# Kernel tuning notes

Measured on AMD Instinct MI355X. Metric: run time of the kernel, lower is better.

## Reference

```python
import jax, jax.numpy as jnp
import numpy as np

SIG = [1, 1, 1, 1, -1]  # Cl(4,1)
NVEC = 5
GA = 1 << NVEC  # 32


def _build_gp_table():
    # Cayley table for the geometric product on blades indexed by bitmask.
    G = np.zeros((GA, GA, GA), np.float32)
    for a in range(GA):
        for b in range(GA):
            s = 0
            t = a >> 1
            while t:
                s += bin(t & b).count('1')
                t >>= 1
            sign = -1.0 if (s & 1) else 1.0
            common = a & b
            for i in range(NVEC):
                if (common >> i) & 1:
                    sign *= SIG[i]
            G[a, b, a ^ b] = sign
    return G

GP_TABLE = jnp.asarray(_build_gp_table())


def geometric_product(x, y):
    return jnp.einsum('...i,...j,ijk->...k', x, y, GP_TABLE)


def manifold_norm(x):
    # normalize each multivector onto the unit sphere in R^32
    return x / (jnp.linalg.norm(x, axis=-1, keepdims=True) + 1e-6)


def versor_linear(x, W, b):
    # channel mixing shared across multivector components: x [..., in, ga]
    return jnp.einsum('...ig,oi->...og', x, W) + b


def layer_norm2d(x, w, b):
    # LayerNorm over last two dims [D, ga] jointly
    mu = jnp.mean(x, axis=(-2, -1), keepdims=True)
    var = jnp.var(x, axis=(-2, -1), keepdims=True)
    return (x - mu) / jnp.sqrt(var + 1e-5) * w + b


def attention(x, Wq, bq, Wk, bk, Wv, bv, Wo, bo, n_heads):
    B, S, D, G = x.shape
    dh = D // n_heads
    q = versor_linear(x, Wq, bq).reshape(B, S, n_heads, dh, G)
    k = versor_linear(x, Wk, bk).reshape(B, S, n_heads, dh, G)
    v = versor_linear(x, Wv, bv).reshape(B, S, n_heads, dh, G)
    scale = 1.0 / np.sqrt(dh * G).astype(np.float32)
    scores = jnp.einsum('bshdg,bthdg->bhst', q, k) * scale
    probs = jax.nn.softmax(scores, axis=-1)
    o = jnp.einsum('bhst,bthdg->bshdg', probs, v).reshape(B, S, D, G)
    return versor_linear(o, Wo, bo)


N_HEADS = 8


def forward(x, Wq, bq, Wk, bk, Wv, bv, Wo, bo, ln1_w, ln1_b, ln2_w, ln2_b,
            gamma1, gamma2, W1, b1, W2, b2, Wr, br, Wc, bc):
    L = Wq.shape[0]
    for l in range(L):
        h = attention(layer_norm2d(x, ln1_w[l], ln1_b[l]),
                      Wq[l], bq[l], Wk[l], bk[l], Wv[l], bv[l], Wo[l], bo[l], N_HEADS)
        x = manifold_norm(x + gamma1[l] * h)
        m = versor_linear(layer_norm2d(x, ln2_w[l], ln2_b[l]), W1[l], b1[l])
        m = versor_linear(jnp.tanh(m), W2[l], b2[l])
        x = manifold_norm(x + gamma2[l] * m)
    # RecursiveRotorAccumulator: log(S)-step inclusive scan of rotors
    delta = versor_linear(x, Wr, br)
    rot = 0.5 * delta
    rot = rot.at[..., 0].add(1.0)
    rot = manifold_norm(rot)
    S = x.shape[1]
    step = 1
    while step < S:
        left = rot[:, :-step]
        right = rot[:, step:]
        comb = manifold_norm(geometric_product(right, left))
        rot = jnp.concatenate([rot[:, :step], comb], axis=1)
        step *= 2
    pooled = rot[:, -1]  # [B, D, ga]
    logits = pooled.reshape(pooled.shape[0], -1) @ Wc.T + bc
    return logits


def setup_inputs() -> dict:
    key = jax.random.key(0)
    B, S, D, G, L, NC = 8, 256, 64, GA, 4, 1000
    E = 4 * D  # expansion hidden
    ks = jax.random.split(key, 16)
    sd = 0.02
    inp = {
        'x': jax.random.normal(ks[0], (B, S, D, G), jnp.float32),
        'Wq': jax.random.normal(ks[1], (L, D, D), jnp.float32) * sd,
        'bq': jnp.zeros((L, D, G), jnp.float32),
        'Wk': jax.random.normal(ks[2], (L, D, D), jnp.float32) * sd,
        'bk': jnp.zeros((L, D, G), jnp.float32),
        'Wv': jax.random.normal(ks[3], (L, D, D), jnp.float32) * sd,
        'bv': jnp.zeros((L, D, G), jnp.float32),
        'Wo': jax.random.normal(ks[4], (L, D, D), jnp.float32) * sd,
        'bo': jnp.zeros((L, D, G), jnp.float32),
        'ln1_w': jnp.ones((L, D, G), jnp.float32),
        'ln1_b': jnp.zeros((L, D, G), jnp.float32),
        'ln2_w': jnp.ones((L, D, G), jnp.float32),
        'ln2_b': jnp.zeros((L, D, G), jnp.float32),
        'gamma1': 1e-5 * jnp.ones((L, D, G), jnp.float32),
        'gamma2': 1e-5 * jnp.ones((L, D, G), jnp.float32),
        'W1': jax.random.normal(ks[5], (L, E, D), jnp.float32) * sd,
        'b1': jnp.zeros((L, E, G), jnp.float32),
        'W2': jax.random.normal(ks[6], (L, D, E), jnp.float32) * sd,
        'b2': jnp.zeros((L, D, G), jnp.float32),
        'Wr': jax.random.normal(ks[7], (D, D), jnp.float32) * sd,
        'br': jnp.zeros((D, G), jnp.float32),
        'Wc': jax.random.normal(ks[8], (NC, D * G), jnp.float32) * sd,
        'bc': jnp.zeros((NC,), jnp.float32),
    }
    return inp


def reference(x, Wq, bq, Wk, bk, Wv, bv, Wo, bo, ln1_w, ln1_b, ln2_w, ln2_b,
              gamma1, gamma2, W1, b1, W2, b2, Wr, br, Wc, bc):
    return forward(x, Wq, bq, Wk, bk, Wv, bv, Wo, bo, ln1_w, ln1_b, ln2_w, ln2_b,
                   gamma1, gamma2, W1, b1, W2, b2, Wr, br, Wc, bc)
```

## Files before the change

### kernel.cpp

```cpp
#include <hip/hip_runtime.h>
#include <hip/hip_bf16.h>

constexpr int kB  = 8;
constexpr int kS  = 256;
constexpr int kD  = 64;
constexpr int kG  = 32;
constexpr int kE  = 256;
constexpr int kNH = 8;
constexpr int kHD = 256;
constexpr int kDG = kD * kG;
constexpr int kT  = kB * kS;
constexpr int kNC = 1000;

using bf16x8 = __attribute__((ext_vector_type(8))) short;
using f32x4  = __attribute__((ext_vector_type(4))) float;

__device__ __forceinline__ short f2bf(float f) {
    unsigned u = __float_as_uint(f);
    unsigned r = (u + 0x7FFFu + ((u >> 16) & 1u)) >> 16;
    return (short)r;
}

__device__ __forceinline__ float tanh_fast(float x) {
    float a = fabsf(x);
// ... 60 lines not shown
#pragma unroll
    for (int j = 0; j < 8; j++) {
        float x = xp[tid + j * 256];
        v[j] = x; s += x; ss += x * x;
        int jj = tid + j * 256;
        xf[(jj & 31) * 68 + (jj >> 5)] = x;
    }
    r1[tid] = s; r2[tid] = ss; __syncthreads();
    for (int o = 128; o > 0; o >>= 1) {
        if (tid < o) { r1[tid] += r1[tid + o]; r2[tid] += r2[tid + o]; }
        __syncthreads();
    }
    float mean = r1[0] * (1.f / kDG);
    float var  = r2[0] * (1.f / kDG) - mean * mean;
    float rstd = rsqrtf(var + 1e-5f);
#pragma unroll
    for (int j = 0; j < 8; j++) {
        int jj = tid + j * 256;
        float val = (v[j] - mean) * rstd * w[jj] + b[jj];
        st[(jj & 31) * 72 + (jj >> 5)] = f2bf(val);
    }
    __syncthreads();
    bf16x8 ov = *(const bf16x8*)&st[(tid >> 3) * 72 + (tid & 7) * 8];
    *(bf16x8*)&A[(size_t)t * kDG + tid * 8] = ov;
    const int row = tid >> 3, col = (tid & 7) * 8;
    float* xo = XT + (size_t)t * kDG + tid * 8;
    *(float4*)(xo + 0) = *(const float4*)&xf[row * 68 + col + 0];
    *(float4*)(xo + 4) = *(const float4*)&xf[row * 68 + col + 4];
}

__global__ __launch_bounds__(256) void vlinT_kernel(const float* __restrict__ XT,
                                                    const float* __restrict__ W,
                                                    const float* __restrict__ bias,
                                                    float* __restrict__ OutT) {
    __shared__ float sx[32 * 65];
    __shared__ float sw[kD * kD];
    int t = blockIdx.x, tid = threadIdx.x;
    const float* xp = XT + (size_t)t * kDG;
    for (int j = tid; j < kDG; j += 256) sx[(j >> 6) * 65 + (j & 63)] = xp[j];
    for (int j = tid; j < kD * kD; j += 256) sw[j] = W[j];
    __syncthreads();
    int g = tid & 31, ob = tid >> 5;
    int b = t >> 8, s = t & 255;
    float* op = OutT + ((size_t)b * kD * kS + s) * kG;
    for (int o = ob; o < kD; o += 8) {
        float acc = bias[o * kG + g];
        const float* wr = sw + o * kD;
#pragma unroll
        for (int i = 0; i < kD; i++) acc += wr[i] * sx[g * 65 + i];
        op[(size_t)o * kS * kG + g] = acc;
    }
}

template<bool LAST>
__global__ __launch_bounds__(128, 3) void mega_kernel(
    const unsigned short* __restrict__ O,
    const unsigned short* __restrict__ Woh, const float* __restrict__ boT,
    const float* __restrict__ gm1T,
    const float* __restrict__ ln2wT, const float* __restrict__ ln2bT,
    const unsigned short* __restrict__ W1h, const float* __restrict__ b1T,
    const unsigned short* __restrict__ W2h, const float* __restrict__ b2T,
    const float* __restrict__ gm2T,
    const float* __restrict__ ln1wT, const float* __restrict__ ln1bT,
    float* __restrict__ XT,
    const unsigned short* __restrict__ Wqh, const unsigned short* __restrict__ Wkh,
    const unsigned short* __restrict__ Wvh,
    const float* __restrict__ bqT, const float* __restrict__ bkT,
    const float* __restrict__ bvT,
    unsigned short* __restrict__ Q, unsigned short* __restrict__ K,
    unsigned short* __restrict__ V) {
    constexpr int AS = 72;
    constexpr int MS = 264;
    __shared__ short sA[32 * AS];
    __shared__ short sM[32 * MS];
    __shared__ float sred[4];

    const int tid = threadIdx.x;
    const int w = tid >> 6, lane = tid & 63;
    const int l16 = lane & 15, quad = lane >> 4;
    const int tok = blockIdx.x;
    const size_t tb = (size_t)tok * kDG;

    float xv[2][2][4];
    bf16x8 w1f[8];
    {
        const unsigned short* xp = O + tb;
        bf16x8 bfr[2][2];
#pragma unroll
        for (int c = 0; c < 2; ++c)
#pragma unroll
            for (int nt = 0; nt < 2; ++nt)
                bfr[c][nt] = *(const bf16x8*)&xp[(nt * 16 + l16) * kD + c * 32 + quad * 8];

        f32x4 accW[2][2];
#pragma unroll
        for (int mt = 0; mt < 2; ++mt)
#pragma unroll
            for (int nt = 0; nt < 2; ++nt) accW[mt][nt] = (f32x4){0.f, 0.f, 0.f, 0.f};
#pragma unroll
        for (int mt = 0; mt < 2; ++mt)
#pragma unroll
            for (int c = 0; c < 2; ++c) {
                bf16x8 afr = *(const bf16x8*)&Woh[(w * 32 + mt * 16 + l16) * kD + c * 32 + quad * 8];
#pragma unroll
                for (int nt = 0; nt < 2; ++nt)
                    accW[mt][nt] = __builtin_amdgcn_mfma_f32_16x16x32_bf16(afr, bfr[c][nt], accW[mt][nt], 0, 0, 0);
            }

#pragma unroll
        for (int mt = 0; mt < 4; ++mt)
#pragma unroll
            for (int c = 0; c < 2; ++c)
                w1f[mt * 2 + c] = *(const bf16x8*)&W1h[((w * 8 + mt) * 16 + l16) * kD + c * 32 + quad * 8];

        float s = 0.f, ss = 0.f;
#pragma unroll
        for (int mt = 0; mt < 2; ++mt) {
            int o0 = w * 32 + mt * 16 + quad * 4;
            float vv[2][4];
#pragma unroll
            for (int nt = 0; nt < 2; ++nt) {
                int g = nt * 16 + l16;
                const float4 b4 = *(const float4*)&boT[g * kD + o0];
                const float4 g4 = *(const float4*)&gm1T[g * kD + o0];
                const float4 xi = *(const float4*)&XT[tb + g * kD + o0];
#pragma unroll
                for (int r = 0; r < 4; ++r)
                    vv[nt][r] = (&xi.x)[r] + (&g4.x)[r] * (accW[mt][nt][r] + (&b4.x)[r]);
            }
#pragma unroll
            for (int r = 0; r < 4; ++r) {
                float sq = vv[0][r] * vv[0][r] + vv[1][r] * vv[1][r];
#pragma unroll
                for (int off = 1; off < 16; off <<= 1) sq += __shfl_xor(sq, off, 64);
                float rn = 1.f / (sqrtf(sq) + 1e-6f);
#pragma unroll
                for (int nt = 0; nt < 2; ++nt) {
                    float x = vv[nt][r] * rn;
                    xv[mt][nt][r] = x;
                    s += x; ss = fmaf(x, x, ss);
                }
            }
        }
#pragma unroll
        for (int off = 1; off < 64; off <<= 1) {
            s += __shfl_xor(s, off, 64); ss += __shfl_xor(ss, off, 64);
        }
        if (lane == 0) { sred[w] = s; sred[2 + w] = ss; }
        __syncthreads();
        float st = sred[0] + sred[1], sst = sred[2] + sred[3];
        float mean = st * (1.f / kDG);
        float var  = sst * (1.f / kDG) - mean * mean;
        float rstd = rsqrtf(var + 1e-5f);
#pragma unroll
        for (int mt = 0; mt < 2; ++mt)
#pragma unroll
            for (int nt = 0; nt < 2; ++nt) {
                int g = nt * 16 + l16;
                int o0 = w * 32 + mt * 16 + quad * 4;
                const float4 w4 = *(const float4*)&ln2wT[g * kD + o0];
                const float4 b4 = *(const float4*)&ln2bT[g * kD + o0];
                short4 s4;
#pragma unroll
                for (int r = 0; r < 4; ++r)
                    (&s4.x)[r] = f2bf((xv[mt][nt][r] - mean) * rstd * (&w4.x)[r] + (&b4.x)[r]);
                *(short4*)&sA[g * AS + o0] = s4;
            }
    }
    __syncthreads();

    bf16x8 w2f[16];
    {
        bf16x8 afrA[2][2];
#pragma unroll
        for (int c = 0; c < 2; ++c)
#pragma unroll
            for (int nt = 0; nt < 2; ++nt)
                afrA[c][nt] = *(const bf16x8*)&sA[(nt * 16 + l16) * AS + c * 32 + quad * 8];

        f32x4 acc1[4][2];
#pragma unroll
        for (int mt = 0; mt < 4; ++mt)
#pragma unroll
            for (int nt = 0; nt < 2; ++nt) acc1[mt][nt] = (f32x4){0.f, 0.f, 0.f, 0.f};
#pragma unroll
        for (int mt = 0; mt < 4; ++mt)
#pragma unroll
            for (int c = 0; c < 2; ++c)
#pragma unroll
                for (int nt = 0; nt < 2; ++nt)
                    acc1[mt][nt] = __builtin_amdgcn_mfma_f32_16x16x32_bf16(w1f[mt * 2 + c], afrA[c][nt], acc1[mt][nt], 0, 0, 0);

        bf16x8 w1g[8];
#pragma unroll
        for (int mt = 0; mt < 4; ++mt)
#pragma unroll
            for (int c = 0; c < 2; ++c)
                w1g[mt * 2 + c] = *(const bf16x8*)&W1h[((w * 8 + 4 + mt) * 16 + l16) * kD + c * 32 + quad * 8];

#pragma unroll
        for (int mt = 0; mt < 4; ++mt)
#pragma unroll
            for (int nt = 0; nt < 2; ++nt) {
                int g = nt * 16 + l16;
                int e0 = (w * 8 + mt) * 16 + quad * 4;
                const float4 b4 = *(const float4*)&b1T[g * kE + e0];
                short4 s4;
#pragma unroll
                for (int r = 0; r < 4; ++r)
                    (&s4.x)[r] = f2bf(tanh_fast(acc1[mt][nt][r] + (&b4.x)[r]));
                *(short4*)&sM[g * MS + e0] = s4;
            }

        f32x4 acc1b[4][2];
#pragma unroll
        for (int mt = 0; mt < 4; ++mt)
#pragma unroll
            for (int nt = 0; nt < 2; ++nt) acc1b[mt][nt] = (f32x4){0.f, 0.f, 0.f, 0.f};
#pragma unroll
        for (int mt = 0; mt < 4; ++mt)
#pragma unroll
            for (int c = 0; c < 2; ++c)
#pragma unroll
                for (int nt = 0; nt < 2; ++nt)
                    acc1b[mt][nt] = __builtin_amdgcn_mfma_f32_16x16x32_bf16(w1g[mt * 2 + c], afrA[c][nt], acc1b[mt][nt], 0, 0, 0);

#pragma unroll
        for (int mt = 0; mt < 2; ++mt)
#pragma unroll
            for (int c = 0; c < 8; ++c)
                w2f[mt * 8 + c] = *(const bf16x8*)&W2h[(w * 32 + mt * 16 + l16) * kE + c * 32 + quad * 8];

#pragma unroll
        for (int mt = 0; mt < 4; ++mt)
#pragma unroll
            for (int nt = 0; nt < 2; ++nt) {
                int g = nt * 16 + l16;
                int e0 = (w * 8 + 4 + mt) * 16 + quad * 4;
                const float4 b4 = *(const float4*)&b1T[g * kE + e0];
                short4 s4;
#pragma unroll
                for (int r = 0; r < 4; ++r)
                    (&s4.x)[r] = f2bf(tanh_fast(acc1b[mt][nt][r] + (&b4.x)[r]));
                *(short4*)&sM[g * MS + e0] = s4;
            }
    }
    __syncthreads();

    f32x4 acc2[2][2];
#pragma unroll
    for (int mt = 0; mt < 2; ++mt)
#pragma unroll
        for (int nt = 0; nt < 2; ++nt) acc2[mt][nt] = (f32x4){0.f, 0.f, 0.f, 0.f};
#pragma unroll
    for (int c = 0; c < 8; ++c) {
        bf16x8 bq[2];
#pragma unroll
        for (int nt = 0; nt < 2; ++nt)
            bq[nt] = *(const bf16x8*)&sM[(nt * 16 + l16) * MS + c * 32 + quad * 8];
#pragma unroll
        for (int mt = 0; mt < 2; ++mt)
#pragma unroll
            for (int nt = 0; nt < 2; ++nt)
                acc2[mt][nt] = __builtin_amdgcn_mfma_f32_16x16x32_bf16(w2f[mt * 8 + c], bq[nt], acc2[mt][nt], 0, 0, 0);
    }

    bf16x8 wqf[12];
    if constexpr (!LAST) {
        const unsigned short* Wp[3] = {Wqh, Wkh, Wvh};
#pragma unroll
        for (int m = 0; m < 3; ++m)
#pragma unroll
            for (int mt = 0; mt < 2; ++mt)
#pragma unroll
                for (int c = 0; c < 2; ++c)
                    wqf[m * 4 + mt * 2 + c] = *(const bf16x8*)&Wp[m][(w * 32 + mt * 16 + l16) * kD + c * 32 + quad * 8];
    }

    float yv[2][2][4];
    float s2 = 0.f, ss2 = 0.f;
#pragma unroll
    for (int mt = 0; mt < 2; ++mt) {
        int o0 = w * 32 + mt * 16 + quad * 4;
        float vv[2][4];
#pragma unroll
        for (int nt = 0; nt < 2; ++nt) {
            int g = nt * 16 + l16;
            const float4 b4 = *(const float4*)&b2T[g * kD + o0];
            const float4 g4 = *(const float4*)&gm2T[g * kD + o0];
#pragma unroll
            for (int r = 0; r < 4; ++r)
                vv[nt][r] = xv[mt][nt][r] + (&g4.x)[r] * (acc2[mt][nt][r] + (&b4.x)[r]);
        }
#pragma unroll
        for (int r = 0; r < 4; ++r) {
            float sq = vv[0][r] * vv[0][r] + vv[1][r] * vv[1][r];
#pragma unroll
            for (int off = 1; off < 16; off <<= 1) sq += __shfl_xor(sq, off, 64);
            float rn = 1.f / (sqrtf(sq) + 1e-6f);
#pragma unroll
            for (int nt = 0; nt < 2; ++nt) {
                float x = vv[nt][r] * rn;
                yv[mt][nt][r] = x;
                s2 += x; ss2 = fmaf(x, x, ss2);
            }
        }
#pragma unroll
        for (int nt = 0; nt < 2; ++nt) {
            int g = nt * 16 + l16;
            float4 xo;
#pragma unroll
            for (int r = 0; r < 4; ++r) (&xo.x)[r] = yv[mt][nt][r];
            *(float4*)&XT[tb + g * kD + o0] = xo;
        }
    }
    if constexpr (LAST) return;

#pragma unroll
    for (int off = 1; off < 64; off <<= 1) {
        s2 += __shfl_xor(s2, off, 64); ss2 += __shfl_xor(ss2, off, 64);
    }
    if (lane == 0) { sred[w] = s2; sred[2 + w] = ss2; }
    __syncthreads();
    {
        float st = sred[0] + sred[1], sst = sred[2] + sred[3];
        float mean = st * (1.f / kDG);
        float var  = sst * (1.f / kDG) - mean * mean;
        float rstd = rsqrtf(var + 1e-5f);
#pragma unroll
        for (int mt = 0; mt < 2; ++mt)
#pragma unroll
            for (int nt = 0; nt < 2; ++nt) {
                int g = nt * 16 + l16;
                int o0 = w * 32 + mt * 16 + quad * 4;
                const float4 w4 = *(const float4*)&ln1wT[g * kD + o0];
                const float4 b4 = *(const float4*)&ln1bT[g * kD + o0];
                short4 s4;
#pragma unroll
                for (int r = 0; r < 4; ++r)
                    (&s4.x)[r] = f2bf((yv[mt][nt][r] - mean) * rstd * (&w4.x)[r] + (&b4.x)[r]);
                *(short4*)&sA[g * AS + o0] = s4;
            }
    }
    __syncthreads();

    {
        bf16x8 afrA[2][2];
#pragma unroll
        for (int c = 0; c < 2; ++c)
#pragma unroll
            for (int nt = 0; nt < 2; ++nt)
                afrA[c][nt] = *(const bf16x8*)&sA[(nt * 16 + l16) * AS + c * 32 + quad * 8];

        const float* Bp[3] = {bqT, bkT, bvT};
        unsigned short* Op[3] = {Q, K, V};
#pragma unroll
        for (int m = 0; m < 3; ++m) {
            f32x4 acc3[2][2];
#pragma unroll
            for (int mt = 0; mt < 2; ++mt)
#pragma unroll
                for (int nt = 0; nt < 2; ++nt) acc3[mt][nt] = (f32x4){0.f, 0.f, 0.f, 0.f};
#pragma unroll
            for (int mt = 0; mt < 2; ++mt)
#pragma unroll
                for (int c = 0; c < 2; ++c)
#pragma unroll
                    for (int nt = 0; nt < 2; ++nt)
                        acc3[mt][nt] = __builtin_amdgcn_mfma_f32_16x16x32_bf16(wqf[m * 4 + mt * 2 + c], afrA[c][nt], acc3[mt][nt], 0, 0, 0);
            unsigned short* op = Op[m] + tb;
#pragma unroll
            for (int mt = 0; mt < 2; ++mt)
#pragma unroll
                for (int nt = 0; nt < 2; ++nt) {
                    int g = nt * 16 + l16;
                    int o0 = w * 32 + mt * 16 + quad * 4;
                    const float4 b4 = *(const float4*)&Bp[m][g * kD + o0];
#pragma unroll
                    for (int r = 0; r < 4; ++r)
                        op[(o0 + r) * kG + g] = (unsigned short)f2bf(acc3[mt][nt][r] + (&b4.x)[r]);
                }
        }
    }
}

__global__ __launch_bounds__(256, 3) void gemm_qkv_kernel(
    const unsigned short* __restrict__ X,
    const unsigned short* __restrict__ Wqh, const unsigned short* __restrict__ Wkh,
    const unsigned short* __restrict__ Wvh,
    const float* __restrict__ bqT, const float* __restrict__ bkT, const float* __restrict__ bvT,
    unsigned short* __restrict__ Q, unsigned short* __restrict__ K, unsigned short* __restrict__ V) {
    constexpr int WS = 64 + 8;
    __shared__ short sW[3 * 64 * WS];

    const int tid = threadIdx.x, wave = tid >> 6, lane = tid & 63;
    const int l16 = lane & 15, quad = lane >> 4;
    const int tok = blockIdx.x * 4 + wave;

    const unsigned short* Wp[3] = {Wqh, Wkh, Wvh};
#pragma unroll
    for (int w = 0; w < 3; ++w)
        for (int j = tid * 8; j < 64 * 64; j += 2048) {
            int o = j >> 6, i = j & 63;
            *(bf16x8*)&sW[w * 64 * WS + o * WS + i] = *(const bf16x8*)(Wp[w] + j);
        }

    const unsigned short* xp = X + (size_t)tok * kDG;
    bf16x8 bfr[2][2];
#pragma unroll
    for (int c = 0; c < 2; ++c)
#pragma unroll
        for (int nt = 0; nt < 2; ++nt)
            bfr[c][nt] = *(const bf16x8*)&xp[(nt * 16 + l16) * kD + c * 32 + quad * 8];
    __syncthreads();

    f32x4 acc[3][4][2];
#pragma unroll
    for (int w = 0; w < 3; ++w)
#pragma unroll
        for (int mt = 0; mt < 4; ++mt)
#pragma unroll
            for (int nt = 0; nt < 2; ++nt) acc[w][mt][nt] = (f32x4){0.f, 0.f, 0.f, 0.f};

#pragma unroll
    for (int w = 0; w < 3; ++w)
#pragma unroll
        for (int mt = 0; mt < 4; ++mt)
#pragma unroll
            for (int c = 0; c < 2; ++c) {
                bf16x8 afr = *(const bf16x8*)&sW[w * 64 * WS + (mt * 16 + l16) * WS + c * 32 + quad * 8];
#pragma unroll
                for (int nt = 0; nt < 2; ++nt)
                    acc[w][mt][nt] = __builtin_amdgcn_mfma_f32_16x16x32_bf16(afr, bfr[c][nt], acc[w][mt][nt], 0, 0, 0);
            }

    unsigned short* Op[3] = {Q, K, V};
    const float* Bp[3] = {bqT, bkT, bvT};
#pragma unroll
    for (int w = 0; w < 3; ++w) {
        unsigned short* op = Op[w] + (size_t)tok * kDG;
#pragma unroll
        for (int mt = 0; mt < 4; ++mt)
#pragma unroll
            for (int nt = 0; nt < 2; ++nt) {
                int g = nt * 16 + l16;
                int o0 = mt * 16 + quad * 4;
                const float4 b4 = *(const float4*)&Bp[w][g * kD + o0];
#pragma unroll
                for (int r = 0; r < 4; ++r)
                    op[(o0 + r) * kG + g] = (unsigned short)f2bf(acc[w][mt][nt][r] + (&b4.x)[r]);
            }
    }
}

constexpr int QSTR = 264;
constexpr int VSTR = 40;

__global__ __launch_bounds__(128) void attn_mfma_kernel(const unsigned short* __restrict__ Q,
                                                        const unsigned short* __restrict__ K,
                                                        const unsigned short* __restrict__ V,
                                                        unsigned short* __restrict__ O) {
    __shared__ short sQ[32 * QSTR];
    __shared__ short sKV[2][256 * VSTR];

    const int qt = blockIdx.x, h = blockIdx.y, b = blockIdx.z;
    const int tid = threadIdx.x;
    const int wave = tid >> 6, lane = tid & 63;
    const int l16 = lane & 15, quad = lane >> 4;

    const size_t bh = (size_t)b * kS * kDG + (size_t)h * kHD;

#pragma unroll
    for (int it = 0; it < 8; ++it) {
        int j = it * 1024 + tid * 8;
        int row = j >> 8, col = j & 255;
        *(bf16x8*)&sQ[row * QSTR + col] =
            *(const bf16x8*)(Q + bh + (size_t)(qt * 32 + row) * kDG + col);
    }
#pragma unroll
    for (int it = 0; it < 8; ++it) {
        int j = it * 1024 + tid * 8;
        int row = j >> 8, col = j & 255;
        *(bf16x8*)&sKV[0][row * QSTR + col] =
            *(const bf16x8*)(K + bh + (size_t)row * kDG + col);
    }
    __syncthreads();

    bf16x8 afrag[8];
    {
        int row = wave * 16 + l16;
#pragma unroll
        for (int c = 0; c < 8; ++c)
            afrag[c] = *(const bf16x8*)&sQ[row * QSTR + c * 32 + quad * 8];
    }

    f32x4 acc[16];
#pragma unroll
    for (int i = 0; i < 16; ++i) acc[i] = (f32x4){0.f, 0.f, 0.f, 0.f};

    for (int kt = 0; kt < 8; ++kt) {
        bf16x8 kpre[8];
        if (kt < 7) {
#pragma unroll
            for (int it = 0; it < 8; ++it) {
                int j = it * 1024 + tid * 8;
                int row = j >> 8, col = j & 255;
                kpre[it] = *(const bf16x8*)(K + bh + (size_t)((kt + 1) * 32 + row) * kDG + col);
            }
        }
        const short* kb = sKV[kt & 1];
#pragma unroll
        for (int nt = 0; nt < 2; ++nt) {
            int key = nt * 16 + l16;
            f32x4 a = acc[kt * 2 + nt];
#pragma unroll
            for (int c = 0; c < 8; ++c) {
                bf16x8 bfrag = *(const bf16x8*)&kb[key * QSTR + c * 32 + quad * 8];
                a = __builtin_amdgcn_mfma_f32_16x16x32_bf16(afrag[c], bfrag, a, 0, 0, 0);
            }
            acc[kt * 2 + nt] = a;
        }
        if (kt < 7) {
            short* nb = sKV[(kt + 1) & 1];
#pragma unroll
            for (int it = 0; it < 8; ++it) {
                int j = it * 1024 + tid * 8;
                int row = j >> 8, col = j & 255;
                *(bf16x8*)&nb[row * QSTR + col] = kpre[it];
            }
            __syncthreads();
        }
    }

    float inv[4];
#pragma unroll
    for (int r = 0; r < 4; ++r) {
        float m = -1e30f;
#pragma unroll
        for (int t = 0; t < 16; ++t) m = fmaxf(m, acc[t][r]);
#pragma unroll
        for (int off = 1; off < 16; off <<= 1) m = fmaxf(m, __shfl_xor(m, off, 16));
        float s = 0.f;
#pragma unroll
        for (int t = 0; t < 16; ++t) {
            float p = __expf((acc[t][r] - m) * 0.0625f);
            acc[t][r] = p; s += p;
        }
#pragma unroll
        for (int off = 1; off < 16; off <<= 1) s += __shfl_xor(s, off, 16);
        inv[r] = 1.f / s;
    }

#pragma unroll
    for (int t = 0; t < 16; ++t)
#pragma unroll
        for (int r = 0; r < 4; ++r)
            sQ[(wave * 16 + quad * 4 + r) * QSTR + t * 16 + l16] = f2bf(acc[t][r]);

    {
        const int db = tid & 63, kh = tid >> 6;
        short4 vr[16];
#pragma unroll
        for (int r = 0; r < 16; ++r)
            vr[r] = *(const short4*)(V + bh + (size_t)(kh * 16 + r) * kDG + db * 4);
#pragma unroll
        for (int i = 0; i < 4; ++i)
#pragma unroll
            for (int gq = 0; gq < 4; ++gq) {
                short4 p = make_short4((&vr[gq * 4 + 0].x)[i], (&vr[gq * 4 + 1].x)[i],
                                       (&vr[gq * 4 + 2].x)[i], (&vr[gq * 4 + 3].x)[i]);
                *(short4*)&sKV[0][(db * 4 + i) * VSTR + kh * 16 + gq * 4] = p;
            }
    }
    __syncthreads();

    f32x4 oacc[16];
#pragma unroll
    for (int i = 0; i < 16; ++i) oacc[i] = (f32x4){0.f, 0.f, 0.f, 0.f};

    for (int vt = 0; vt < 8; ++vt) {
        short4 vpre[16];
        if (vt < 7) {
            const int db = tid & 63, kh = tid >> 6;
#pragma unroll
            for (int r = 0; r < 16; ++r)
                vpre[r] = *(const short4*)(V + bh + (size_t)((vt + 1) * 32 + kh * 16 + r) * kDG + db * 4);
        }
        const short* vb = sKV[vt & 1];
        bf16x8 pfrag = *(const bf16x8*)&sQ[(wave * 16 + l16) * QSTR + vt * 32 + quad * 8];
#pragma unroll
        for (int dt = 0; dt < 16; ++dt) {
            bf16x8 vfrag = *(const bf16x8*)&vb[(dt * 16 + l16) * VSTR + quad * 8];
            oacc[dt] = __builtin_amdgcn_mfma_f32_16x16x32_bf16(pfrag, vfrag, oacc[dt], 0, 0, 0);
        }
        if (vt < 7) {
            const int db = tid & 63, kh = tid >> 6;
            short* nb = sKV[(vt + 1) & 1];
#pragma unroll
            for (int i = 0; i < 4; ++i)
#pragma unroll
                for (int gq = 0; gq < 4; ++gq) {
                    short4 p = make_short4((&vpre[gq * 4 + 0].x)[i], (&vpre[gq * 4 + 1].x)[i],
                                           (&vpre[gq * 4 + 2].x)[i], (&vpre[gq * 4 + 3].x)[i]);
                    *(short4*)&nb[(db * 4 + i) * VSTR + kh * 16 + gq * 4] = p;
                }
            __syncthreads();
        }
    }

    {
        const size_t ob = (size_t)(b * kS + qt * 32 + wave * 16 + quad * 4) * kDG + h * 8;
#pragma unroll
        for (int gg = 0; gg < 2; ++gg) {
            int g = gg * 16 + l16;
#pragma unroll
            for (int r = 0; r < 4; ++r) {
                bf16x8 pk;
#pragma unroll
                for (int k = 0; k < 8; ++k)
                    pk[k] = f2bf(oacc[k * 2 + gg][r] * inv[r]);
                *(bf16x8*)&O[ob + (size_t)r * kDG + g * kD] = pk;
            }
        }
    }
}

constexpr int pc_ce(unsigned v) { int c = 0; while (v) { c += v & 1; v >>= 1; } return c; }
constexpr unsigned gp_mask_ce(int a) {
    unsigned m = 0;
    for (int c = 0; c < 32; ++c) {
        int b = a ^ c;
        int s = (a & b) >> 4;
        for (int t = a >> 1; t; t >>= 1) s += pc_ce(t & b);
        if (s & 1) m |= (1u << c);
    }
    return m;
}

template<int A>
__device__ __forceinline__ void gp_term(const float* x, const float* y, float* acc) {
    constexpr unsigned m = gp_mask_ce(A);
    const float xa = x[A], nxa = -xa;
#pragma unroll
    for (int c = 0; c < 32; ++c)
        acc[c] = fmaf(((m >> c) & 1u) ? nxa : xa, y[A ^ c], acc[c]);
}

__device__ __forceinline__ void gp_mn_t(const float* x, const float* y, float* out) {
    float acc[32];
#pragma unroll
    for (int c = 0; c < 32; ++c) acc[c] = 0.f;
    gp_term<0>(x, y, acc);  gp_term<1>(x, y, acc);  gp_term<2>(x, y, acc);  gp_term<3>(x, y, acc);
    gp_term<4>(x, y, acc);  gp_term<5>(x, y, acc);  gp_term<6>(x, y, acc);  gp_term<7>(x, y, acc);
    gp_term<8>(x, y, acc);  gp_term<9>(x, y, acc);  gp_term<10>(x, y, acc); gp_term<11>(x, y, acc);
    gp_term<12>(x, y, acc); gp_term<13>(x, y, acc); gp_term<14>(x, y, acc); gp_term<15>(x, y, acc);
    gp_term<16>(x, y, acc); gp_term<17>(x, y, acc); gp_term<18>(x, y, acc); gp_term<19>(x, y, acc);
    gp_term<20>(x, y, acc); gp_term<21>(x, y, acc); gp_term<22>(x, y, acc); gp_term<23>(x, y, acc);
    gp_term<24>(x, y, acc); gp_term<25>(x, y, acc); gp_term<26>(x, y, acc); gp_term<27>(x, y, acc);
// ... 75 lines not shown
    for (int cc = 0; cc < 8; ++cc) {
        const float4 w4 = *(const float4*)(w + cc * 256 + lane * 4);
#pragma unroll
        for (int b = 0; b < kB; ++b) {
            const float4 p4 = *(const float4*)&sp[b * kDG + cc * 256 + lane * 4];
            acc[b] += w4.x * p4.x + w4.y * p4.y + w4.z * p4.z + w4.w * p4.w;
        }
    }
#pragma unroll
    for (int b = 0; b < kB; ++b)
#pragma unroll
        for (int off = 32; off > 0; off >>= 1) acc[b] += __shfl_xor(acc[b], off, 64);
    if (lane == 0) {
        float bias = bc[c];
#pragma unroll
        for (int b = 0; b < kB; ++b) out[b * kNC + c] = acc[b] + bias;
    }
}

extern "C" void kernel_launch(void* const* d_in, const int* in_sizes, int n_in,
                              void* d_out, int out_size, void* d_ws, size_t ws_size,
                              hipStream_t stream) {
    const float* x_in = (const float*)d_in[0];
    const float* Wq   = (const float*)d_in[1];
    const float* bq   = (const float*)d_in[2];
    const float* Wk   = (const float*)d_in[3];
    const float* bk   = (const float*)d_in[4];
    const float* Wv   = (const float*)d_in[5];
    const float* bv   = (const float*)d_in[6];
    const float* Wo   = (const float*)d_in[7];
    const float* bo   = (const float*)d_in[8];
    const float* ln1w = (const float*)d_in[9];
    const float* ln1b = (const float*)d_in[10];
    const float* ln2w = (const float*)d_in[11];
    const float* ln2b = (const float*)d_in[12];
    const float* gm1  = (const float*)d_in[13];
    const float* gm2  = (const float*)d_in[14];
    const float* W1   = (const float*)d_in[15];
    const float* b1   = (const float*)d_in[16];
    const float* W2   = (const float*)d_in[17];
    const float* b2   = (const float*)d_in[18];
    const float* Wr   = (const float*)d_in[19];
    const float* br   = (const float*)d_in[20];
    const float* Wc   = (const float*)d_in[21];
    const float* bc   = (const float*)d_in[22];

    const size_t NEL = (size_t)kT * kDG;
    float* F  = (float*)d_ws;
    float* XT = F;
    unsigned short* Abf = (unsigned short*)(F + NEL);
    unsigned short* Qh = (unsigned short*)(F + 2 * NEL);
    unsigned short* Kh = (unsigned short*)(F + 3 * NEL);
    unsigned short* Vh = (unsigned short*)(F + 4 * NEL);
    unsigned short* Wb = (unsigned short*)(F + 5 * NEL);
    float* PT = F + 3 * NEL + NEL / 2;
    float* pooled = F + 2 * NEL;
    float* DT = F + NEL;

    cvtw_kernel<<<192, 256, 0, stream>>>(Wq, Wk, Wv, Wo, W1, W2, Wb);
    prep_tr_kernel<<<48, 256, 0, stream>>>(bq, bk, bv, bo, b2, gm1, gm2,
                                           ln2w, ln2b, ln1w, ln1b, b1, PT);
    unsigned short* Wqh = Wb;
    unsigned short* Wkh = Wb + 16384;
    unsigned short* Wvh = Wb + 32768;
    unsigned short* Woh = Wb + 49152;
    unsigned short* W1h = Wb + 65536;
    unsigned short* W2h = Wb + 131072;

    auto bqT   = [&](int l) { return PT + 0     + l * 2048; };
    auto bkT   = [&](int l) { return PT + 8192  + l * 2048; };
    auto bvT   = [&](int l) { return PT + 16384 + l * 2048; };
    auto boT   = [&](int l) { return PT + 24576 + l * 2048; };
    auto b2T   = [&](int l) { return PT + 32768 + l * 2048; };
    auto gm1T  = [&](int l) { return PT + 40960 + l * 2048; };
    auto gm2T  = [&](int l) { return PT + 49152 + l * 2048; };
    auto ln2wT = [&](int l) { return PT + 57344 + l * 2048; };
    auto ln2bT = [&](int l) { return PT + 65536 + l * 2048; };
    auto ln1wT = [&](int l) { return PT + 73728 + l * 2048; };
    auto ln1bT = [&](int l) { return PT + 81920 + l * 2048; };
    auto b1T   = [&](int l) { return PT + 90112 + l * 8192; };

    ln_kernel<<<kT, 256, 0, stream>>>(x_in, ln1w, ln1b, Abf, XT);
    gemm_qkv_kernel<<<kT / 4, 256, 0, stream>>>(Abf,
        Wqh, Wkh, Wvh, bqT(0), bkT(0), bvT(0), Qh, Kh, Vh);

    for (int l = 0; l < 4; l++) {
        attn_mfma_kernel<<<dim3(8, kNH, kB), 128, 0, stream>>>(Qh, Kh, Vh, Abf);
        if (l < 3)
            mega_kernel<false><<<kT, 128, 0, stream>>>(Abf,
                Woh + l * 4096, boT(l), gm1T(l), ln2wT(l), ln2bT(l),
                W1h + l * 16384, b1T(l), W2h + l * 16384, b2T(l), gm2T(l),
                ln1wT(l + 1), ln1bT(l + 1), XT,
                Wqh + (l + 1) * 4096, Wkh + (l + 1) * 4096, Wvh + (l + 1) * 4096,
                bqT(l + 1), bkT(l + 1), bvT(l + 1), Qh, Kh, Vh);
        else
            mega_kernel<true><<<kT, 128, 0, stream>>>(Abf,
                Woh + l * 4096, boT(l), gm1T(l), ln2wT(l), ln2bT(l),
                W1h + l * 16384, b1T(l), W2h + l * 16384, b2T(l), gm2T(l),
                nullptr, nullptr, XT,
                nullptr, nullptr, nullptr, nullptr, nullptr, nullptr,
                nullptr, nullptr, nullptr);
    }

    vlinT_kernel<<<kT, 256, 0, stream>>>(XT, Wr, br, DT);
    scanreg_kernel<<<kB * kD / 4, 256, 0, stream>>>(DT, pooled);
    cls2_kernel<<<kNC / 4, 256, 0, stream>>>(pooled, Wc, bc, (float*)d_out);
}
```

Before: 530.2 us.

## Pre-transpose V in separate kernel and widen mega_kernel to four waves

Adds a vtr_kernel that writes V in a per-head transposed [d][s] layout after each QKV projection. The attention kernel can then load V tiles with contiguous 16-byte loads instead of strided short4 gathers with an in-register transpose. Separately, mega_kernel now runs with 256 threads per block, four waves each owning 16 output rows, which lowers per-thread register use and raises parallelism per token. The cost is an extra launch and an extra read and write of V per layer, plus more block-level synchronisation across four waves.

```diff
diff --git a/kernel.cpp b/kernel.cpp
--- a/kernel.cpp
+++ b/kernel.cpp
@@ -136,8 +136,38 @@
     }
 }
 
+__global__ __launch_bounds__(128) void vtr_kernel(const unsigned short* __restrict__ V,
+                                                  unsigned short* __restrict__ VT) {
+    __shared__ short ts[32 * 264];
+    const int s = blockIdx.x, h = blockIdx.y, b = blockIdx.z;
+    const int tid = threadIdx.x;
+    const unsigned short* src = V + ((size_t)(b * kS + s * 32)) * kDG + h * kHD;
+#pragma unroll
+    for (int it = 0; it < 8; ++it) {
+        int j = it * 1024 + tid * 8;
+        int row = j >> 8, col = j & 255;
+        *(bf16x8*)&ts[row * 264 + col] = *(const bf16x8*)(src + (size_t)row * kDG + col);
+    }
+    __syncthreads();
+    unsigned short* dst = VT + ((size_t)(b * kNH + h) * 256) * 256;
+#pragma unroll
+    for (int half = 0; half < 2; ++half) {
+        int d = half * 128 + tid;
+        short v[32];
+#pragma unroll
+        for (int k = 0; k < 32; ++k) v[k] = ts[k * 264 + d];
+#pragma unroll
+        for (int c2 = 0; c2 < 4; ++c2) {
+            bf16x8 pk;
+#pragma unroll
+            for (int j = 0; j < 8; ++j) pk[j] = v[c2 * 8 + j];
+            *(bf16x8*)(dst + (size_t)d * 256 + s * 32 + c2 * 8) = pk;
+        }
+    }
+}
+
 template<bool LAST>
-__global__ __launch_bounds__(128, 3) void mega_kernel(
+__global__ __launch_bounds__(256, 2) void mega_kernel(
     const unsigned short* __restrict__ O,
     const unsigned short* __restrict__ Woh, const float* __restrict__ boT,
     const float* __restrict__ gm1T,
@@ -157,15 +187,16 @@
     constexpr int MS = 264;
     __shared__ short sA[32 * AS];
     __shared__ short sM[32 * MS];
-    __shared__ float sred[4];
+    __shared__ float sred[8];
 
     const int tid = threadIdx.x;
     const int w = tid >> 6, lane = tid & 63;
     const int l16 = lane & 15, quad = lane >> 4;
     const int tok = blockIdx.x;
     const size_t tb = (size_t)tok * kDG;
-
-    float xv[2][2][4];
+    const int o0 = w * 16 + quad * 4;
+
+    float xv[2][4];
     bf16x8 w1f[8];
     {
         const unsigned short* xp = O + tb;
@@ -176,118 +207,105 @@
             for (int nt = 0; nt < 2; ++nt)
                 bfr[c][nt] = *(const bf16x8*)&xp[(nt * 16 + l16) * kD + c * 32 + quad * 8];
 
-        f32x4 accW[2][2];
-#pragma unroll
-        for (int mt = 0; mt < 2; ++mt)
-#pragma unroll
-            for (int nt = 0; nt < 2; ++nt) accW[mt][nt] = (f32x4){0.f, 0.f, 0.f, 0.f};
-#pragma unroll
-        for (int mt = 0; mt < 2; ++mt)
-#pragma unroll
-            for (int c = 0; c < 2; ++c) {
-                bf16x8 afr = *(const bf16x8*)&Woh[(w * 32 + mt * 16 + l16) * kD + c * 32 + quad * 8];
-#pragma unroll
-                for (int nt = 0; nt < 2; ++nt)
-                    accW[mt][nt] = __builtin_amdgcn_mfma_f32_16x16x32_bf16(afr, bfr[c][nt], accW[mt][nt], 0, 0, 0);
-            }
+        f32x4 accW[2];
+#pragma unroll
+        for (int nt = 0; nt < 2; ++nt) accW[nt] = (f32x4){0.f, 0.f, 0.f, 0.f};
+#pragma unroll
+        for (int c = 0; c < 2; ++c) {
+            bf16x8 afr = *(const bf16x8*)&Woh[(w * 16 + l16) * kD + c * 32 + quad * 8];
+#pragma unroll
+            for (int nt = 0; nt < 2; ++nt)
+                accW[nt] = __builtin_amdgcn_mfma_f32_16x16x32_bf16(afr, bfr[c][nt], accW[nt], 0, 0, 0);
+        }
 
 #pragma unroll
         for (int mt = 0; mt < 4; ++mt)
 #pragma unroll
             for (int c = 0; c < 2; ++c)
-                w1f[mt * 2 + c] = *(const bf16x8*)&W1h[((w * 8 + mt) * 16 + l16) * kD + c * 32 + quad * 8];
+                w1f[mt * 2 + c] = *(const bf16x8*)&W1h[((w * 4 + mt) * 16 + l16) * kD + c * 32 + quad * 8];
 
         float s = 0.f, ss = 0.f;
-#pragma unroll
-        for (int mt = 0; mt < 2; ++mt) {
-            int o0 = w * 32 + mt * 16 + quad * 4;
-            float vv[2][4];
+        float vv[2][4];
+#pragma unroll
+        for (int nt = 0; nt < 2; ++nt) {
+            int g = nt * 16 + l16;
+            const float4 b4 = *(const float4*)&boT[g * kD + o0];
+            const float4 g4 = *(const float4*)&gm1T[g * kD + o0];
+            const float4 xi = *(const float4*)&XT[tb + g * kD + o0];
+#pragma unroll
+            for (int r = 0; r < 4; ++r)
+                vv[nt][r] = (&xi.x)[r] + (&g4.x)[r] * (accW[nt][r] + (&b4.x)[r]);
+        }
+#pragma unroll
+        for (int r = 0; r < 4; ++r) {
+            float sq = vv[0][r] * vv[0][r] + vv[1][r] * vv[1][r];
+#pragma unroll
+            for (int off = 1; off < 16; off <<= 1) sq += __shfl_xor(sq, off, 64);
+            float rn = 1.f / (sqrtf(sq) + 1e-6f);
 #pragma unroll
             for (int nt = 0; nt < 2; ++nt) {
-                int g = nt * 16 + l16;
-                const float4 b4 = *(const float4*)&boT[g * kD + o0];
-                const float4 g4 = *(const float4*)&gm1T[g * kD + o0];
-                const float4 xi = *(const float4*)&XT[tb + g * kD + o0];
-#pragma unroll
-                for (int r = 0; r < 4; ++r)
-                    vv[nt][r] = (&xi.x)[r] + (&g4.x)[r] * (accW[mt][nt][r] + (&b4.x)[r]);
-            }
-#pragma unroll
-            for (int r = 0; r < 4; ++r) {
-                float sq = vv[0][r] * vv[0][r] + vv[1][r] * vv[1][r];
-#pragma unroll
-                for (int off = 1; off < 16; off <<= 1) sq += __shfl_xor(sq, off, 64);
-                float rn = 1.f / (sqrtf(sq) + 1e-6f);
-#pragma unroll
-                for (int nt = 0; nt < 2; ++nt) {
-                    float x = vv[nt][r] * rn;
-                    xv[mt][nt][r] = x;
-                    s += x; ss = fmaf(x, x, ss);
-                }
+                float x = vv[nt][r] * rn;
+                xv[nt][r] = x;
+                s += x; ss = fmaf(x, x, ss);
             }
         }
 #pragma unroll
         for (int off = 1; off < 64; off <<= 1) {
             s += __shfl_xor(s, off, 64); ss += __shfl_xor(ss, off, 64);
         }
-        if (lane == 0) { sred[w] = s; sred[2 + w] = ss; }
+        if (lane == 0) { sred[w] = s; sred[4 + w] = ss; }
         __syncthreads();
-        float st = sred[0] + sred[1], sst = sred[2] + sred[3];
+        float st = sred[0] + sred[1] + sred[2] + sred[3];
+        float sst = sred[4] + sred[5] + sred[6] + sred[7];
         float mean = st * (1.f / kDG);
         float var  = sst * (1.f / kDG) - mean * mean;
         float rstd = rsqrtf(var + 1e-5f);
 #pragma unroll
-        for (int mt = 0; mt < 2; ++mt)
+        for (int nt = 0; nt < 2; ++nt) {
+            int g = nt * 16 + l16;
+            const float4 w4 = *(const float4*)&ln2wT[g * kD + o0];
+            const float4 b4 = *(const float4*)&ln2bT[g * kD + o0];
+            short4 s4;
+#pragma unroll
+            for (int r = 0; r < 4; ++r)
+                (&s4.x)[r] = f2bf((xv[nt][r] - mean) * rstd * (&w4.x)[r] + (&b4.x)[r]);
+            *(short4*)&sA[g * AS + o0] = s4;
+        }
+    }
+    __syncthreads();
+
+    bf16x8 w2f[8];
+    {
+        bf16x8 afrA[2][2];
+#pragma unroll
+        for (int c = 0; c < 2; ++c)
+#pragma unroll
+            for (int nt = 0; nt < 2; ++nt)
+                afrA[c][nt] = *(const bf16x8*)&sA[(nt * 16 + l16) * AS + c * 32 + quad * 8];
+
+        f32x4 acc1[4][2];
+#pragma unroll
+        for (int mt = 0; mt < 4; ++mt)
+#pragma unroll
+            for (int nt = 0; nt < 2; ++nt) acc1[mt][nt] = (f32x4){0.f, 0.f, 0.f, 0.f};
+#pragma unroll
+        for (int mt = 0; mt < 4; ++mt)
+#pragma unroll
+            for (int c = 0; c < 2; ++c)
+#pragma unroll
+                for (int nt = 0; nt < 2; ++nt)
+                    acc1[mt][nt] = __builtin_amdgcn_mfma_f32_16x16x32_bf16(w1f[mt * 2 + c], afrA[c][nt], acc1[mt][nt], 0, 0, 0);
+
+#pragma unroll
+        for (int c = 0; c < 8; ++c)
+            w2f[c] = *(const bf16x8*)&W2h[(w * 16 + l16) * kE + c * 32 + quad * 8];
+
+#pragma unroll
+        for (int mt = 0; mt < 4; ++mt)
 #pragma unroll
             for (int nt = 0; nt < 2; ++nt) {
                 int g = nt * 16 + l16;
-                int o0 = w * 32 + mt * 16 + quad * 4;
-                const float4 w4 = *(const float4*)&ln2wT[g * kD + o0];
-                const float4 b4 = *(const float4*)&ln2bT[g * kD + o0];
-                short4 s4;
-#pragma unroll
-                for (int r = 0; r < 4; ++r)
-                    (&s4.x)[r] = f2bf((xv[mt][nt][r] - mean) * rstd * (&w4.x)[r] + (&b4.x)[r]);
-                *(short4*)&sA[g * AS + o0] = s4;
-            }
-    }
-    __syncthreads();
-
-    bf16x8 w2f[16];
-    {
-        bf16x8 afrA[2][2];
-#pragma unroll
-        for (int c = 0; c < 2; ++c)
-#pragma unroll
-            for (int nt = 0; nt < 2; ++nt)
-                afrA[c][nt] = *(const bf16x8*)&sA[(nt * 16 + l16) * AS + c * 32 + quad * 8];
-
-        f32x4 acc1[4][2];
-#pragma unroll
-        for (int mt = 0; mt < 4; ++mt)
-#pragma unroll
-            for (int nt = 0; nt < 2; ++nt) acc1[mt][nt] = (f32x4){0.f, 0.f, 0.f, 0.f};
-#pragma unroll
-        for (int mt = 0; mt < 4; ++mt)
-#pragma unroll
-            for (int c = 0; c < 2; ++c)
-#pragma unroll
-                for (int nt = 0; nt < 2; ++nt)
-                    acc1[mt][nt] = __builtin_amdgcn_mfma_f32_16x16x32_bf16(w1f[mt * 2 + c], afrA[c][nt], acc1[mt][nt], 0, 0, 0);
-
-        bf16x8 w1g[8];
-#pragma unroll
-        for (int mt = 0; mt < 4; ++mt)
-#pragma unroll
-            for (int c = 0; c < 2; ++c)
-                w1g[mt * 2 + c] = *(const bf16x8*)&W1h[((w * 8 + 4 + mt) * 16 + l16) * kD + c * 32 + quad * 8];
-
-#pragma unroll
-        for (int mt = 0; mt < 4; ++mt)
-#pragma unroll
-            for (int nt = 0; nt < 2; ++nt) {
-                int g = nt * 16 + l16;
-                int e0 = (w * 8 + mt) * 16 + quad * 4;
+                int e0 = (w * 4 + mt) * 16 + quad * 4;
                 const float4 b4 = *(const float4*)&b1T[g * kE + e0];
                 short4 s4;
 #pragma unroll
@@ -295,47 +313,12 @@
                     (&s4.x)[r] = f2bf(tanh_fast(acc1[mt][nt][r] + (&b4.x)[r]));
                 *(short4*)&sM[g * MS + e0] = s4;
             }
-
-        f32x4 acc1b[4][2];
-#pragma unroll
-        for (int mt = 0; mt < 4; ++mt)
-#pragma unroll
-            for (int nt = 0; nt < 2; ++nt) acc1b[mt][nt] = (f32x4){0.f, 0.f, 0.f, 0.f};
-#pragma unroll
-        for (int mt = 0; mt < 4; ++mt)
-#pragma unroll
-            for (int c = 0; c < 2; ++c)
-#pragma unroll
-                for (int nt = 0; nt < 2; ++nt)
-                    acc1b[mt][nt] = __builtin_amdgcn_mfma_f32_16x16x32_bf16(w1g[mt * 2 + c], afrA[c][nt], acc1b[mt][nt], 0, 0, 0);
-
-#pragma unroll
-        for (int mt = 0; mt < 2; ++mt)
-#pragma unroll
-            for (int c = 0; c < 8; ++c)
-                w2f[mt * 8 + c] = *(const bf16x8*)&W2h[(w * 32 + mt * 16 + l16) * kE + c * 32 + quad * 8];
-
-#pragma unroll
-        for (int mt = 0; mt < 4; ++mt)
-#pragma unroll
-            for (int nt = 0; nt < 2; ++nt) {
-                int g = nt * 16 + l16;
-                int e0 = (w * 8 + 4 + mt) * 16 + quad * 4;
-                const float4 b4 = *(const float4*)&b1T[g * kE + e0];
-                short4 s4;
-#pragma unroll
-                for (int r = 0; r < 4; ++r)
-                    (&s4.x)[r] = f2bf(tanh_fast(acc1b[mt][nt][r] + (&b4.x)[r]));
-                *(short4*)&sM[g * MS + e0] = s4;
-            }
-    }
-    __syncthreads();
-
-    f32x4 acc2[2][2];
-#pragma unroll
-    for (int mt = 0; mt < 2; ++mt)
-#pragma unroll
-        for (int nt = 0; nt < 2; ++nt) acc2[mt][nt] = (f32x4){0.f, 0.f, 0.f, 0.f};
+    }
+    __syncthreads();
+
+    f32x4 acc2[2];
+#pragma unroll
+    for (int nt = 0; nt < 2; ++nt) acc2[nt] = (f32x4){0.f, 0.f, 0.f, 0.f};
 #pragma unroll
     for (int c = 0; c < 8; ++c) {
         bf16x8 bq[2];
@@ -343,29 +326,23 @@
         for (int nt = 0; nt < 2; ++nt)
             bq[nt] = *(const bf16x8*)&sM[(nt * 16 + l16) * MS + c * 32 + quad * 8];
 #pragma unroll
-        for (int mt = 0; mt < 2; ++mt)
-#pragma unroll
-            for (int nt = 0; nt < 2; ++nt)
-                acc2[mt][nt] = __builtin_amdgcn_mfma_f32_16x16x32_bf16(w2f[mt * 8 + c], bq[nt], acc2[mt][nt], 0, 0, 0);
-    }
-
-    bf16x8 wqf[12];
+        for (int nt = 0; nt < 2; ++nt)
+            acc2[nt] = __builtin_amdgcn_mfma_f32_16x16x32_bf16(w2f[c], bq[nt], acc2[nt], 0, 0, 0);
+    }
+
+    bf16x8 wqf[6];
     if constexpr (!LAST) {
         const unsigned short* Wp[3] = {Wqh, Wkh, Wvh};
 #pragma unroll
         for (int m = 0; m < 3; ++m)
 #pragma unroll
-            for (int mt = 0; mt < 2; ++mt)
-#pragma unroll
-                for (int c = 0; c < 2; ++c)
-                    wqf[m * 4 + mt * 2 + c] = *(const bf16x8*)&Wp[m][(w * 32 + mt * 16 + l16) * kD + c * 32 + quad * 8];
-    }
-
-    float yv[2][2][4];
+            for (int c = 0; c < 2; ++c)
+                wqf[m * 2 + c] = *(const bf16x8*)&Wp[m][(w * 16 + l16) * kD + c * 32 + quad * 8];
+    }
+
+    float yv[2][4];
     float s2 = 0.f, ss2 = 0.f;
-#pragma unroll
-    for (int mt = 0; mt < 2; ++mt) {
-        int o0 = w * 32 + mt * 16 + quad * 4;
+    {
         float vv[2][4];
 #pragma unroll
         for (int nt = 0; nt < 2; ++nt) {
@@ -374,7 +351,7 @@
             const float4 g4 = *(const float4*)&gm2T[g * kD + o0];
 #pragma unroll
             for (int r = 0; r < 4; ++r)
-                vv[nt][r] = xv[mt][nt][r] + (&g4.x)[r] * (acc2[mt][nt][r] + (&b4.x)[r]);
+                vv[nt][r] = xv[nt][r] + (&g4.x)[r] * (acc2[nt][r] + (&b4.x)[r]);
         }
 #pragma unroll
         for (int r = 0; r < 4; ++r) {
@@ -385,7 +362,7 @@
 #pragma unroll
             for (int nt = 0; nt < 2; ++nt) {
                 float x = vv[nt][r] * rn;
-                yv[mt][nt][r] = x;
+                yv[nt][r] = x;
                 s2 += x; ss2 = fmaf(x, x, ss2);
             }
         }
@@ -394,7 +371,7 @@
             int g = nt * 16 + l16;
             float4 xo;
 #pragma unroll
-            for (int r = 0; r < 4; ++r) (&xo.x)[r] = yv[mt][nt][r];
+            for (int r = 0; r < 4; ++r) (&xo.x)[r] = yv[nt][r];
             *(float4*)&XT[tb + g * kD + o0] = xo;
         }
     }
@@ -404,66 +381,57 @@
     for (int off = 1; off < 64; off <<= 1) {
         s2 += __shfl_xor(s2, off, 64); ss2 += __shfl_xor(ss2, off, 64);
     }
-    if (lane == 0) { sred[w] = s2; sred[2 + w] = ss2; }
+    if (lane == 0) { sred[w] = s2; sred[4 + w] = ss2; }
     __syncthreads();
     {
-        float st = sred[0] + sred[1], sst = sred[2] + sred[3];
+        float st = sred[0] + sred[1] + sred[2] + sred[3];
+        float sst = sred[4] + sred[5] + sred[6] + sred[7];
         float mean = st * (1.f / kDG);
         float var  = sst * (1.f / kDG) - mean * mean;
         float rstd = rsqrtf(var + 1e-5f);
 #pragma unroll
-        for (int mt = 0; mt < 2; ++mt)
+        for (int nt = 0; nt < 2; ++nt) {
+            int g = nt * 16 + l16;
+            const float4 w4 = *(const float4*)&ln1wT[g * kD + o0];
+            const float4 b4 = *(const float4*)&ln1bT[g * kD + o0];
+            short4 s4;
+#pragma unroll
+            for (int r = 0; r < 4; ++r)
+                (&s4.x)[r] = f2bf((yv[nt][r] - mean) * rstd * (&w4.x)[r] + (&b4.x)[r]);
+            *(short4*)&sA[g * AS + o0] = s4;
+        }
+    }
+    __syncthreads();
+
+    {
+        bf16x8 afrA[2][2];
+#pragma unroll
+        for (int c = 0; c < 2; ++c)
+#pragma unroll
+            for (int nt = 0; nt < 2; ++nt)
+                afrA[c][nt] = *(const bf16x8*)&sA[(nt * 16 + l16) * AS + c * 32 + quad * 8];
+
+        const float* Bp[3] = {bqT, bkT, bvT};
+        unsigned short* Op[3] = {Q, K, V};
+#pragma unroll
+        for (int m = 0; m < 3; ++m) {
+            f32x4 acc3[2];
+#pragma unroll
+            for (int nt = 0; nt < 2; ++nt) acc3[nt] = (f32x4){0.f, 0.f, 0.f, 0.f};
+#pragma unroll
+            for (int c = 0; c < 2; ++c)
+#pragma unroll
+                for (int nt = 0; nt < 2; ++nt)
+                    acc3[nt] = __builtin_amdgcn_mfma_f32_16x16x32_bf16(wqf[m * 2 + c], afrA[c][nt], acc3[nt], 0, 0, 0);
+            unsigned short* op = Op[m] + tb;
 #pragma unroll
             for (int nt = 0; nt < 2; ++nt) {
                 int g = nt * 16 + l16;
-                int o0 = w * 32 + mt * 16 + quad * 4;
-                const float4 w4 = *(const float4*)&ln1wT[g * kD + o0];
-                const float4 b4 = *(const float4*)&ln1bT[g * kD + o0];
-                short4 s4;
+                const float4 b4 = *(const float4*)&Bp[m][g * kD + o0];
 #pragma unroll
                 for (int r = 0; r < 4; ++r)
-                    (&s4.x)[r] = f2bf((yv[mt][nt][r] - mean) * rstd * (&w4.x)[r] + (&b4.x)[r]);
-                *(short4*)&sA[g * AS + o0] = s4;
-            }
-    }
-    __syncthreads();
-
-    {
-        bf16x8 afrA[2][2];
-#pragma unroll
-        for (int c = 0; c < 2; ++c)
-#pragma unroll
-            for (int nt = 0; nt < 2; ++nt)
-                afrA[c][nt] = *(const bf16x8*)&sA[(nt * 16 + l16) * AS + c * 32 + quad * 8];
-
-        const float* Bp[3] = {bqT, bkT, bvT};
-        unsigned short* Op[3] = {Q, K, V};
-#pragma unroll
-        for (int m = 0; m < 3; ++m) {
-            f32x4 acc3[2][2];
-#pragma unroll
-            for (int mt = 0; mt < 2; ++mt)
-#pragma unroll
-                for (int nt = 0; nt < 2; ++nt) acc3[mt][nt] = (f32x4){0.f, 0.f, 0.f, 0.f};
-#pragma unroll
-            for (int mt = 0; mt < 2; ++mt)
-#pragma unroll
-                for (int c = 0; c < 2; ++c)
-#pragma unroll
-                    for (int nt = 0; nt < 2; ++nt)
-                        acc3[mt][nt] = __builtin_amdgcn_mfma_f32_16x16x32_bf16(wqf[m * 4 + mt * 2 + c], afrA[c][nt], acc3[mt][nt], 0, 0, 0);
-            unsigned short* op = Op[m] + tb;
-#pragma unroll
-            for (int mt = 0; mt < 2; ++mt)
-#pragma unroll
-                for (int nt = 0; nt < 2; ++nt) {
-                    int g = nt * 16 + l16;
-                    int o0 = w * 32 + mt * 16 + quad * 4;
-                    const float4 b4 = *(const float4*)&Bp[m][g * kD + o0];
-#pragma unroll
-                    for (int r = 0; r < 4; ++r)
-                        op[(o0 + r) * kG + g] = (unsigned short)f2bf(acc3[mt][nt][r] + (&b4.x)[r]);
-                }
+                    op[(o0 + r) * kG + g] = (unsigned short)f2bf(acc3[nt][r] + (&b4.x)[r]);
+            }
         }
     }
 }
@@ -542,7 +510,7 @@
 
 __global__ __launch_bounds__(128) void attn_mfma_kernel(const unsigned short* __restrict__ Q,
                                                         const unsigned short* __restrict__ K,
-                                                        const unsigned short* __restrict__ V,
+                                                        const unsigned short* __restrict__ VT,
                                                         unsigned short* __restrict__ O) {
     __shared__ short sQ[32 * QSTR];
     __shared__ short sKV[2][256 * VSTR];
@@ -553,6 +521,7 @@
     const int l16 = lane & 15, quad = lane >> 4;
 
     const size_t bh = (size_t)b * kS * kDG + (size_t)h * kHD;
+    const unsigned short* VTp = VT + (size_t)(b * kNH + h) * 256 * 256;
 
 #pragma unroll
     for (int it = 0; it < 8; ++it) {
@@ -641,20 +610,11 @@
         for (int r = 0; r < 4; ++r)
             sQ[(wave * 16 + quad * 4 + r) * QSTR + t * 16 + l16] = f2bf(acc[t][r]);
 
-    {
-        const int db = tid & 63, kh = tid >> 6;
-        short4 vr[16];
-#pragma unroll
-        for (int r = 0; r < 16; ++r)
-            vr[r] = *(const short4*)(V + bh + (size_t)(kh * 16 + r) * kDG + db * 4);
-#pragma unroll
-        for (int i = 0; i < 4; ++i)
-#pragma unroll
-            for (int gq = 0; gq < 4; ++gq) {
-                short4 p = make_short4((&vr[gq * 4 + 0].x)[i], (&vr[gq * 4 + 1].x)[i],
-                                       (&vr[gq * 4 + 2].x)[i], (&vr[gq * 4 + 3].x)[i]);
-                *(short4*)&sKV[0][(db * 4 + i) * VSTR + kh * 16 + gq * 4] = p;
-            }
+#pragma unroll
+    for (int it = 0; it < 8; ++it) {
+        int j = it * 128 + tid;
+        int d = j >> 2, q4 = (j & 3) * 8;
+        *(bf16x8*)&sKV[0][d * VSTR + q4] = *(const bf16x8*)(VTp + (size_t)d * 256 + q4);
     }
     __syncthreads();
 
@@ -663,12 +623,14 @@
     for (int i = 0; i < 16; ++i) oacc[i] = (f32x4){0.f, 0.f, 0.f, 0.f};
 
     for (int vt = 0; vt < 8; ++vt) {
-        short4 vpre[16];
+        bf16x8 vpre[8];
         if (vt < 7) {
-            const int db = tid & 63, kh = tid >> 6;
-#pragma unroll
-            for (int r = 0; r < 16; ++r)
-                vpre[r] = *(const short4*)(V + bh + (size_t)((vt + 1) * 32 + kh * 16 + r) * kDG + db * 4);
+#pragma unroll
+            for (int it = 0; it < 8; ++it) {
+                int j = it * 128 + tid;
+                int d = j >> 2, q4 = (j & 3) * 8;
+                vpre[it] = *(const bf16x8*)(VTp + (size_t)d * 256 + (vt + 1) * 32 + q4);
+            }
         }
         const short* vb = sKV[vt & 1];
         bf16x8 pfrag = *(const bf16x8*)&sQ[(wave * 16 + l16) * QSTR + vt * 32 + quad * 8];
@@ -678,16 +640,13 @@
             oacc[dt] = __builtin_amdgcn_mfma_f32_16x16x32_bf16(pfrag, vfrag, oacc[dt], 0, 0, 0);
         }
         if (vt < 7) {
-            const int db = tid & 63, kh = tid >> 6;
             short* nb = sKV[(vt + 1) & 1];
 #pragma unroll
-            for (int i = 0; i < 4; ++i)
-#pragma unroll
-                for (int gq = 0; gq < 4; ++gq) {
-                    short4 p = make_short4((&vpre[gq * 4 + 0].x)[i], (&vpre[gq * 4 + 1].x)[i],
-                                           (&vpre[gq * 4 + 2].x)[i], (&vpre[gq * 4 + 3].x)[i]);
-                    *(short4*)&nb[(db * 4 + i) * VSTR + kh * 16 + gq * 4] = p;
-                }
+            for (int it = 0; it < 8; ++it) {
+                int j = it * 128 + tid;
+                int d = j >> 2, q4 = (j & 3) * 8;
+                *(bf16x8*)&nb[d * VSTR + q4] = vpre[it];
+            }
             __syncthreads();
         }
     }
@@ -869,6 +828,7 @@
     unsigned short* Qh = (unsigned short*)(F + 2 * NEL);
     unsigned short* Kh = (unsigned short*)(F + 3 * NEL);
     unsigned short* Vh = (unsigned short*)(F + 4 * NEL);
+    unsigned short* VT = (unsigned short*)(F + 4 * NEL + NEL / 2);
     unsigned short* Wb = (unsigned short*)(F + 5 * NEL);
     float* PT = F + 3 * NEL + NEL / 2;
     float* pooled = F + 2 * NEL;
@@ -900,23 +860,26 @@
     ln_kernel<<<kT, 256, 0, stream>>>(x_in, ln1w, ln1b, Abf, XT);
     gemm_qkv_kernel<<<kT / 4, 256, 0, stream>>>(Abf,
         Wqh, Wkh, Wvh, bqT(0), bkT(0), bvT(0), Qh, Kh, Vh);
+    vtr_kernel<<<dim3(8, kNH, kB), 128, 0, stream>>>(Vh, VT);
 
     for (int l = 0; l < 4; l++) {
-        attn_mfma_kernel<<<dim3(8, kNH, kB), 128, 0, stream>>>(Qh, Kh, Vh, Abf);
-        if (l < 3)
-            mega_kernel<false><<<kT, 128, 0, stream>>>(Abf,
+        attn_mfma_kernel<<<dim3(8, kNH, kB), 128, 0, stream>>>(Qh, Kh, VT, Abf);
+        if (l < 3) {
+            mega_kernel<false><<<kT, 256, 0, stream>>>(Abf,
                 Woh + l * 4096, boT(l), gm1T(l), ln2wT(l), ln2bT(l),
                 W1h + l * 16384, b1T(l), W2h + l * 16384, b2T(l), gm2T(l),
                 ln1wT(l + 1), ln1bT(l + 1), XT,
                 Wqh + (l + 1) * 4096, Wkh + (l + 1) * 4096, Wvh + (l + 1) * 4096,
                 bqT(l + 1), bkT(l + 1), bvT(l + 1), Qh, Kh, Vh);
-        else
-            mega_kernel<true><<<kT, 128, 0, stream>>>(Abf,
+            vtr_kernel<<<dim3(8, kNH, kB), 128, 0, stream>>>(Vh, VT);
+        } else {
+            mega_kernel<true><<<kT, 256, 0, stream>>>(Abf,
                 Woh + l * 4096, boT(l), gm1T(l), ln2wT(l), ln2bT(l),
                 W1h + l * 16384, b1T(l), W2h + l * 16384, b2T(l), gm2T(l),
                 nullptr, nullptr, XT,
                 nullptr, nullptr, nullptr, nullptr, nullptr, nullptr,
                 nullptr, nullptr, nullptr);
+        }
     }
 
     vlinT_kernel<<<kT, 256, 0, stream>>>(XT, Wr, br, DT);
```

Result: no change. 538.7 us (+1.6%).
